# Kernel optimization log

Measured on AMD Instinct MI355X. Metric: run time of the kernel, lower is better.

## Reference

```python
import jax, jax.numpy as jnp
import numpy as np

B, N, H = 2, 2048, 256
NUM_HEADS = 8
HEAD_DIM = H // NUM_HEADS
E = 65536
NEG = -1e30
LN_EPS = 1e-5


def setup_inputs() -> dict:
    key = jax.random.key(0)
    ks = jax.random.split(key, 8)
    x = jax.random.normal(ks[0], (B, N, H), dtype=jnp.float32)
    edge_index = jax.random.randint(ks[1], (2, E), 0, N, dtype=jnp.int32)
    edge_weights = jax.random.uniform(ks[2], (E,), dtype=jnp.float32)
    s = 1.0 / np.sqrt(H)
    Wq = jax.random.normal(ks[3], (H, H), dtype=jnp.float32) * s
    Wk = jax.random.normal(ks[4], (H, H), dtype=jnp.float32) * s
    Wv = jax.random.normal(ks[5], (H, H), dtype=jnp.float32) * s
    Wo = jax.random.normal(ks[6], (H, H), dtype=jnp.float32) * s
    ln_gamma = jnp.ones((H,), dtype=jnp.float32)
    ln_beta = jnp.zeros((H,), dtype=jnp.float32)
    return {"node_embeddings": x, "edge_index": edge_index, "edge_weights": edge_weights,
            "Wq": Wq, "Wk": Wk, "Wv": Wv, "Wo": Wo, "ln_gamma": ln_gamma, "ln_beta": ln_beta}


def reference(node_embeddings, edge_index, edge_weights, Wq, Wk, Wv, Wo, ln_gamma, ln_beta):
    x = node_embeddings
    residual = x
    # torch Linear: y = x @ W.T
    def proj(W):
        y = jnp.einsum('bnd,ed->bne', x, W)
        return y.reshape(B, N, NUM_HEADS, HEAD_DIM).transpose(0, 2, 1, 3)  # [B,h,N,hd]
    Q, K, V = proj(Wq), proj(Wk), proj(Wv)
    scale = 1.0 / jnp.sqrt(jnp.float32(HEAD_DIM))
    scores = jnp.einsum('bhnd,bhmd->bhnm', Q, K) * scale  # [B,h,N,N]
    # adjacency mask from edge list
    mask = jnp.zeros((N, N), dtype=bool).at[edge_index[0], edge_index[1]].set(True)
    scores = jnp.where(mask[None, None], scores, NEG)
    w = jax.nn.softmax(scores, axis=-1)
    # rows with no edges: softmax over uniform NEG -> uniform; multiply by mask zeroes them
    # (equivalent to torch's -inf softmax + nan->0, but grad-safe)
    w = w * mask[None, None].astype(w.dtype)
    attn = jnp.einsum('bhnm,bhmd->bhnd', w, V)
    attn = attn.transpose(0, 2, 1, 3).reshape(B, N, H)
    out = jnp.einsum('bnd,ed->bne', attn, Wo)
    y = out + residual
    mu = jnp.mean(y, axis=-1, keepdims=True)
    var = jnp.mean(jnp.square(y - mu), axis=-1, keepdims=True)
    y = (y - mu) / jnp.sqrt(var + LN_EPS) * ln_gamma + ln_beta
    return y
```

## Files before the change

kernel.cpp:

```cpp
#include <hip/hip_runtime.h>
#include <math.h>

#define Bb 2
#define Nn 2048
#define Hh 256
#define NH 8
#define HD 32
#define NEDGE 65536
#define LN_EPS 1e-5f
#define MW 64

typedef __bf16 bf16_t;
typedef bf16_t bf16x8 __attribute__((ext_vector_type(8)));
typedef bf16_t bf16x4 __attribute__((ext_vector_type(4)));
typedef float f32x4 __attribute__((ext_vector_type(4)));

__global__ void build_mask_kernel(const int* __restrict__ ei, unsigned int* __restrict__ mask) {
    int e = blockIdx.x * blockDim.x + threadIdx.x;
    if (e >= NEDGE) return;
    int src = ei[e];
    int dst = ei[NEDGE + e];
    atomicOr(&mask[src * MW + (dst >> 5)], 1u << (dst & 31));
}

__global__ __launch_bounds__(256) void cvt_zero_kernel(
    const float* __restrict__ s0, const float* __restrict__ s1, const float* __restrict__ s2,
    const float* __restrict__ s3, const float* __restrict__ s4,
    bf16_t* __restrict__ d0, bf16_t* __restrict__ d1, bf16_t* __restrict__ d2,
    bf16_t* __restrict__ d3, bf16_t* __restrict__ d4,
    uint4* __restrict__ mask4)
{
    int which = blockIdx.y;
    int i = blockIdx.x * blockDim.x + threadIdx.x;
    if (which == 5) {
        if (i < Nn * MW / 4) mask4[i] = make_uint4(0, 0, 0, 0);
        return;
    }
    const float* s = (which == 0) ? s0 : (which == 1) ? s1 : (which == 2) ? s2 : (which == 3) ? s3 : s4;
    bf16_t* d = (which == 0) ? d0 : (which == 1) ? d1 : (which == 2) ? d2 : (which == 3) ? d3 : d4;
    int n4 = (which == 0) ? (Bb * Nn * Hh / 4) : (Hh * Hh / 4);
    if (i >= n4) return;
    float4 v = ((const float4*)s)[i];
    bf16x4 o = {(bf16_t)v.x, (bf16_t)v.y, (bf16_t)v.z, (bf16_t)v.w};
    ((bf16x4*)d)[i] = o;
}

#define LDA2 72

__global__ __launch_bounds__(256) void qkv_gemm3_kernel(
    const bf16_t* __restrict__ xb,
    const bf16_t* __restrict__ Wqb, const bf16_t* __restrict__ Wkb, const bf16_t* __restrict__ Wvb,
    float* __restrict__ Qb, bf16_t* __restrict__ Kb16, bf16_t* __restrict__ Vb16)
{
    __shared__ bf16_t As[64 * LDA2];
    __shared__ bf16_t Ws[64 * LDA2];
    int t = threadIdx.x;
    int lane = t & 63, w = t >> 6;
    int wm = w & 1, wn = w >> 1;
    int ml = lane & 15, quad = lane >> 4;
    int m0 = blockIdx.x * 64;
    int wsel = blockIdx.y >> 2;
    const bf16_t* W = (wsel == 0) ? Wqb : ((wsel == 1) ? Wkb : Wvb);
    int n0 = (blockIdx.y & 3) * 64;
    int srow = t >> 3;
    int scol = (t & 7) * 8;
    f32x4 acc[2][2];
    f32x4 zero = {0.f, 0.f, 0.f, 0.f};
    acc[0][0] = zero; acc[0][1] = zero; acc[1][0] = zero; acc[1][1] = zero;

    for (int k0 = 0; k0 < Hh; k0 += 64) {
        bf16x8 a[2], b[2];
        #pragma unroll
        for (int s = 0; s < 2; ++s) {
            a[s] = *(const bf16x8*)(xb + (size_t)(m0 + srow + s * 32) * Hh + k0 + scol);
            b[s] = *(const bf16x8*)(W  + (size_t)(n0 + srow + s * 32) * Hh + k0 + scol);
        }
        __syncthreads();
        #pragma unroll
        for (int s = 0; s < 2; ++s) {
            *(bf16x8*)&As[(srow + s * 32) * LDA2 + scol] = a[s];
            *(bf16x8*)&Ws[(srow + s * 32) * LDA2 + scol] = b[s];
        }
        __syncthreads();
        #pragma unroll
        for (int kk = 0; kk < 64; kk += 32) {
            bf16x8 af[2], bfr[2];
            #pragma unroll
            for (int i = 0; i < 2; ++i) {
                af[i]  = *(const bf16x8*)&As[(wm * 32 + i * 16 + ml) * LDA2 + kk + quad * 8];
                bfr[i] = *(const bf16x8*)&Ws[(wn * 32 + i * 16 + ml) * LDA2 + kk + quad * 8];
            }
            #pragma unroll
            for (int i = 0; i < 2; ++i)
                #pragma unroll
                for (int j = 0; j < 2; ++j)
                    acc[i][j] = __builtin_amdgcn_mfma_f32_16x16x32_bf16(af[i], bfr[j], acc[i][j], 0, 0, 0);
        }
    }
    bf16_t* Ob16 = (wsel == 1) ? Kb16 : Vb16;
    #pragma unroll
    for (int i = 0; i < 2; ++i)
        #pragma unroll
        for (int j = 0; j < 2; ++j)
            #pragma unroll
            for (int r = 0; r < 4; ++r) {
                int mg = m0 + wm * 32 + i * 16 + quad * 4 + r;
                int ng = n0 + wn * 32 + j * 16 + ml;
                float v = acc[i][j][r];
                if (wsel == 0) Qb[(size_t)mg * Hh + ng] = v;
                else           Ob16[(size_t)mg * Hh + ng] = (bf16_t)v;
            }
}

__global__ __launch_bounds__(256) void attn5_kernel(
    const float* __restrict__ Qb, const bf16_t* __restrict__ Kb16, const bf16_t* __restrict__ Vb16,
    const unsigned int* __restrict__ mask, float* __restrict__ attnb)
{
    __shared__ unsigned short nbr[Nn];
    __shared__ float qs[Hh];
    __shared__ float sraw[32 * 9];
    __shared__ float scw[Hh];
    __shared__ float alpha_l[NH];
    __shared__ float linv_l[NH];
    __shared__ float obuf[4][Hh];
    __shared__ int nn_sh;
    int gid = blockIdx.x;
    int i = gid & (Nn - 1);
    int b = gid >> 11;
    int t = threadIdx.x;
    int h = t >> 5, dl = t & 31;
    int w = t >> 6, lane = t & 63;
    int hw = lane >> 3;

    if (t < 64) {
        unsigned int bits = mask[i * MW + t];
        int cnt = __popc(bits);
        int incl = cnt;
        #pragma unroll
        for (int off = 1; off < 64; off <<= 1) {
            int v = __shfl_up(incl, off, 64);
            if (t >= off) incl += v;
        }
        int idx = incl - cnt;
        unsigned int bb = bits;
        while (bb) {
            int bit = __ffs(bb) - 1;
            nbr[idx++] = (unsigned short)(t * 32 + bit);
            bb &= bb - 1;
        }
        if (t == 63) nn_sh = incl;
    }
    qs[t] = Qb[((size_t)((b << 11) + i)) * Hh + t];
    __syncthreads();
    int nn = nn_sh;

    float m_run = -1e30f, l_run = 0.f;
    float o0 = 0.f, o1 = 0.f, o2 = 0.f, o3 = 0.f;
    const float scale = 0.17677669529663687f;
    int nch = (nn + 31) >> 5;
    for (int c = 0; c < nch; ++c) {
        int base = c << 5;
        int lim = min(32, nn - base);
        float4 qv = *(const float4*)&qs[lane << 2];
        #pragma unroll
        for (int s = 0; s < 8; ++s) {
            int r = (s << 2) + w;
            if (r < lim) {
                int j = nbr[base + r];
                bf16x4 kv = *(const bf16x4*)(Kb16 + (((size_t)((b << 11) + j)) << 8) + (lane << 2));
                float p = fmaf((float)kv.x, qv.x, fmaf((float)kv.y, qv.y,
                          fmaf((float)kv.z, qv.z, (float)kv.w * qv.w)));
                p += __shfl_xor(p, 1, 64);
                p += __shfl_xor(p, 2, 64);
                p += __shfl_xor(p, 4, 64);
                if ((lane & 7) == 0) sraw[r * 9 + (lane >> 3)] = p * scale;
            }
        }
        __syncthreads();
        float s_val = (dl < lim) ? sraw[dl * 9 + h] : -1e30f;
        float mc = s_val;
        #pragma unroll
        for (int m = 1; m < 32; m <<= 1) mc = fmaxf(mc, __shfl_xor(mc, m, 64));
        float m_new = fmaxf(m_run, mc);
        float wgt = __expf(s_val - m_new);
        float sum = wgt;
        #pragma unroll
        for (int m = 1; m < 32; m <<= 1) sum += __shfl_xor(sum, m, 64);
        float alpha = __expf(m_run - m_new);
        l_run = l_run * alpha + sum;
        m_run = m_new;
        scw[t] = wgt;
        if (dl == 0) alpha_l[h] = alpha;
        __syncthreads();
        float av = alpha_l[hw];
        o0 *= av; o1 *= av; o2 *= av; o3 *= av;
        #pragma unroll
        for (int s = 0; s < 8; ++s) {
            int r = (s << 2) + w;
            if (r < lim) {
                int j = nbr[base + r];
                float wg = scw[(hw << 5) + r];
                bf16x4 vv = *(const bf16x4*)(Vb16 + (((size_t)((b << 11) + j)) << 8) + (lane << 2));
                o0 = fmaf(wg, (float)vv.x, o0);
                o1 = fmaf(wg, (float)vv.y, o1);
                o2 = fmaf(wg, (float)vv.z, o2);
                o3 = fmaf(wg, (float)vv.w, o3);
            }
        }
    }
    if (dl == 0) linv_l[h] = (l_run > 0.f) ? 1.f / l_run : 0.f;
    obuf[w][(lane << 2) + 0] = o0;
    obuf[w][(lane << 2) + 1] = o1;
    obuf[w][(lane << 2) + 2] = o2;
    obuf[w][(lane << 2) + 3] = o3;
    __syncthreads();
    float val = obuf[0][t] + obuf[1][t] + obuf[2][t] + obuf[3][t];
    attnb[(((size_t)((b << 11) + i)) << 8) + t] = val * linv_l[t >> 5];
}

__global__ __launch_bounds__(256) void out_ln_kernel(
    const float* __restrict__ attnb, const bf16_t* __restrict__ Wob,
    const float* __restrict__ x, const float* __restrict__ gamma,
    const float* __restrict__ beta, float* __restrict__ out)
{
    __shared__ bf16_t As[16 * LDA2];
    __shared__ __align__(16) char wbuf[256 * LDA2 * sizeof(bf16_t)];
    bf16_t* Ws = (bf16_t*)wbuf;
    float* yb = (float*)wbuf;
    int t = threadIdx.x;
    int lane = t & 63, w = t >> 6;
    int ml = lane & 15, quad = lane >> 4;
    int m0 = blockIdx.x * 16;
    f32x4 acc[4];
    f32x4 zero = {0.f, 0.f, 0.f, 0.f};
    acc[0] = zero; acc[1] = zero; acc[2] = zero; acc[3] = zero;
    int arow = t >> 4, acol = (t & 15) * 4;
    int wrow = t >> 3, wcol = (t & 7) * 8;

    for (int k0 = 0; k0 < Hh; k0 += 64) {
        float4 av = *(const float4*)(attnb + (size_t)(m0 + arow) * Hh + k0 + acol);
        bf16x8 wv[8];
        #pragma unroll
        for (int s = 0; s < 8; ++s)
            wv[s] = *(const bf16x8*)(Wob + (size_t)(wrow + s * 32) * Hh + k0 + wcol);
        __syncthreads();
        bf16x4 ac = {(bf16_t)av.x, (bf16_t)av.y, (bf16_t)av.z, (bf16_t)av.w};
        *(bf16x4*)&As[arow * LDA2 + acol] = ac;
        #pragma unroll
        for (int s = 0; s < 8; ++s)
            *(bf16x8*)&Ws[(wrow + s * 32) * LDA2 + wcol] = wv[s];
        __syncthreads();
        #pragma unroll
        for (int kk = 0; kk < 64; kk += 32) {
            bf16x8 af = *(const bf16x8*)&As[ml * LDA2 + kk + quad * 8];
            #pragma unroll
            for (int ct = 0; ct < 4; ++ct) {
                bf16x8 bfr = *(const bf16x8*)&Ws[(w * 64 + ct * 16 + ml) * LDA2 + kk + quad * 8];
                acc[ct] = __builtin_amdgcn_mfma_f32_16x16x32_bf16(af, bfr, acc[ct], 0, 0, 0);
            }
        }
    }
    __syncthreads();
    #pragma unroll
    for (int ct = 0; ct < 4; ++ct)
        #pragma unroll
        for (int r = 0; r < 4; ++r) {
            int row = quad * 4 + r;
            int col = w * 64 + ct * 16 + ml;
            yb[row * 260 + col] = acc[ct][r] + x[(size_t)(m0 + row) * Hh + col];
        }
    __syncthreads();
    for (int rr = 0; rr < 4; ++rr) {
        int row = w * 4 + rr;
        float4 v = *(const float4*)&yb[row * 260 + lane * 4];
        float sum = v.x + v.y + v.z + v.w;
        #pragma unroll
        for (int m = 1; m < 64; m <<= 1) sum += __shfl_xor(sum, m, 64);
        float mu = sum * (1.f / Hh);
        float4 d = {v.x - mu, v.y - mu, v.z - mu, v.w - mu};
        float ss = d.x * d.x + d.y * d.y + d.z * d.z + d.w * d.w;
        #pragma unroll
        for (int m = 1; m < 64; m <<= 1) ss += __shfl_xor(ss, m, 64);
        float r = rsqrtf(ss * (1.f / Hh) + LN_EPS);
        float4 g  = *(const float4*)(gamma + lane * 4);
        float4 bt = *(const float4*)(beta + lane * 4);
        float4 ov = {d.x * r * g.x + bt.x, d.y * r * g.y + bt.y,
                     d.z * r * g.z + bt.z, d.w * r * g.w + bt.w};
        *(float4*)(out + (size_t)(m0 + row) * Hh + lane * 4) = ov;
    }
}

extern "C" void kernel_launch(void* const* d_in, const int* in_sizes, int n_in,
                              void* d_out, int out_size, void* d_ws, size_t ws_size,
                              hipStream_t stream) {
    const float* x     = (const float*)d_in[0];
    const int*   ei    = (const int*)d_in[1];
    const float* Wq    = (const float*)d_in[3];
    const float* Wk    = (const float*)d_in[4];
    const float* Wv    = (const float*)d_in[5];
    const float* Wo    = (const float*)d_in[6];
    const float* gamma = (const float*)d_in[7];
    const float* beta  = (const float*)d_in[8];
    float* out = (float*)d_out;

    const int NTOK = Bb * Nn * Hh;
    float*  Qb    = (float*)d_ws;
    bf16_t* Kb16  = (bf16_t*)(Qb + NTOK);
    bf16_t* Vb16  = Kb16 + NTOK;
    float*  attnb = (float*)(Vb16 + NTOK);
    unsigned int* mask = (unsigned int*)(attnb + NTOK);
    bf16_t* xb  = (bf16_t*)(mask + Nn * MW);
    bf16_t* Wqb = xb + NTOK;
    bf16_t* Wkb = Wqb + Hh * Hh;
    bf16_t* Wvb = Wkb + Hh * Hh;
    bf16_t* Wob = Wvb + Hh * Hh;

    hipLaunchKernelGGL(cvt_zero_kernel, dim3(NTOK / 4 / 256, 6), dim3(256), 0, stream,
                       x, Wq, Wk, Wv, Wo, xb, Wqb, Wkb, Wvb, Wob, (uint4*)mask);
    hipLaunchKernelGGL(build_mask_kernel, dim3(NEDGE / 256), dim3(256), 0, stream, ei, mask);
    hipLaunchKernelGGL(qkv_gemm3_kernel, dim3((Bb * Nn) / 64, 12), dim3(256), 0, stream,
                       xb, Wqb, Wkb, Wvb, Qb, Kb16, Vb16);
    hipLaunchKernelGGL(attn5_kernel, dim3(Bb * Nn), dim3(256), 0, stream,
                       Qb, Kb16, Vb16, mask, attnb);
    hipLaunchKernelGGL(out_ln_kernel, dim3((Bb * Nn) / 16), dim3(256), 0, stream,
                       attnb, Wob, x, gamma, beta, out);
}
```

Measured before the change: 117.4 us.

## Fuse bf16 conversion into GEMMs and process both batches per attention block

Removes the separate fp32-to-bf16 conversion kernel. The QKV and output GEMMs now load fp32 inputs and convert them while staging into shared memory, and the mask is cleared with a memset. The attention kernel now handles both batch elements for a node in one block, so the neighbour list is built once and reused, and the grid is halved. The cost is more registers and shared memory per attention block, and fp32 global loads that are twice as wide inside the GEMMs.

```diff
diff --git a/kernel.cpp b/kernel.cpp
--- a/kernel.cpp
+++ b/kernel.cpp
@@ -23,33 +23,11 @@
     atomicOr(&mask[src * MW + (dst >> 5)], 1u << (dst & 31));
 }
 
-__global__ __launch_bounds__(256) void cvt_zero_kernel(
-    const float* __restrict__ s0, const float* __restrict__ s1, const float* __restrict__ s2,
-    const float* __restrict__ s3, const float* __restrict__ s4,
-    bf16_t* __restrict__ d0, bf16_t* __restrict__ d1, bf16_t* __restrict__ d2,
-    bf16_t* __restrict__ d3, bf16_t* __restrict__ d4,
-    uint4* __restrict__ mask4)
-{
-    int which = blockIdx.y;
-    int i = blockIdx.x * blockDim.x + threadIdx.x;
-    if (which == 5) {
-        if (i < Nn * MW / 4) mask4[i] = make_uint4(0, 0, 0, 0);
-        return;
-    }
-    const float* s = (which == 0) ? s0 : (which == 1) ? s1 : (which == 2) ? s2 : (which == 3) ? s3 : s4;
-    bf16_t* d = (which == 0) ? d0 : (which == 1) ? d1 : (which == 2) ? d2 : (which == 3) ? d3 : d4;
-    int n4 = (which == 0) ? (Bb * Nn * Hh / 4) : (Hh * Hh / 4);
-    if (i >= n4) return;
-    float4 v = ((const float4*)s)[i];
-    bf16x4 o = {(bf16_t)v.x, (bf16_t)v.y, (bf16_t)v.z, (bf16_t)v.w};
-    ((bf16x4*)d)[i] = o;
-}
-
 #define LDA2 72
 
 __global__ __launch_bounds__(256) void qkv_gemm3_kernel(
-    const bf16_t* __restrict__ xb,
-    const bf16_t* __restrict__ Wqb, const bf16_t* __restrict__ Wkb, const bf16_t* __restrict__ Wvb,
+    const float* __restrict__ x,
+    const float* __restrict__ Wq, const float* __restrict__ Wk, const float* __restrict__ Wv,
     float* __restrict__ Qb, bf16_t* __restrict__ Kb16, bf16_t* __restrict__ Vb16)
 {
     __shared__ bf16_t As[64 * LDA2];
@@ -60,7 +38,7 @@
     int ml = lane & 15, quad = lane >> 4;
     int m0 = blockIdx.x * 64;
     int wsel = blockIdx.y >> 2;
-    const bf16_t* W = (wsel == 0) ? Wqb : ((wsel == 1) ? Wkb : Wvb);
+    const float* W = (wsel == 0) ? Wq : ((wsel == 1) ? Wk : Wv);
     int n0 = (blockIdx.y & 3) * 64;
     int srow = t >> 3;
     int scol = (t & 7) * 8;
@@ -69,17 +47,25 @@
     acc[0][0] = zero; acc[0][1] = zero; acc[1][0] = zero; acc[1][1] = zero;
 
     for (int k0 = 0; k0 < Hh; k0 += 64) {
-        bf16x8 a[2], b[2];
+        float4 a[2][2], bwt[2][2];
         #pragma unroll
         for (int s = 0; s < 2; ++s) {
-            a[s] = *(const bf16x8*)(xb + (size_t)(m0 + srow + s * 32) * Hh + k0 + scol);
-            b[s] = *(const bf16x8*)(W  + (size_t)(n0 + srow + s * 32) * Hh + k0 + scol);
+            const float* ap = x + (size_t)(m0 + srow + s * 32) * Hh + k0 + scol;
+            a[s][0] = *(const float4*)ap;
+            a[s][1] = *(const float4*)(ap + 4);
+            const float* bp = W + (size_t)(n0 + srow + s * 32) * Hh + k0 + scol;
+            bwt[s][0] = *(const float4*)bp;
+            bwt[s][1] = *(const float4*)(bp + 4);
         }
         __syncthreads();
         #pragma unroll
         for (int s = 0; s < 2; ++s) {
-            *(bf16x8*)&As[(srow + s * 32) * LDA2 + scol] = a[s];
-            *(bf16x8*)&Ws[(srow + s * 32) * LDA2 + scol] = b[s];
+            bf16x8 av = {(bf16_t)a[s][0].x, (bf16_t)a[s][0].y, (bf16_t)a[s][0].z, (bf16_t)a[s][0].w,
+                         (bf16_t)a[s][1].x, (bf16_t)a[s][1].y, (bf16_t)a[s][1].z, (bf16_t)a[s][1].w};
+            bf16x8 bv = {(bf16_t)bwt[s][0].x, (bf16_t)bwt[s][0].y, (bf16_t)bwt[s][0].z, (bf16_t)bwt[s][0].w,
+                         (bf16_t)bwt[s][1].x, (bf16_t)bwt[s][1].y, (bf16_t)bwt[s][1].z, (bf16_t)bwt[s][1].w};
+            *(bf16x8*)&As[(srow + s * 32) * LDA2 + scol] = av;
+            *(bf16x8*)&Ws[(srow + s * 32) * LDA2 + scol] = bv;
         }
         __syncthreads();
         #pragma unroll
@@ -112,21 +98,19 @@
             }
 }
 
-__global__ __launch_bounds__(256) void attn5_kernel(
+__global__ __launch_bounds__(256) void attn6_kernel(
     const float* __restrict__ Qb, const bf16_t* __restrict__ Kb16, const bf16_t* __restrict__ Vb16,
     const unsigned int* __restrict__ mask, float* __restrict__ attnb)
 {
     __shared__ unsigned short nbr[Nn];
-    __shared__ float qs[Hh];
-    __shared__ float sraw[32 * 9];
-    __shared__ float scw[Hh];
-    __shared__ float alpha_l[NH];
-    __shared__ float linv_l[NH];
+    __shared__ float qs[2][Hh];
+    __shared__ float sraw[2][32 * 9];
+    __shared__ float scw[2][Hh];
+    __shared__ float alpha_l[2][NH];
+    __shared__ float linv_l[2][NH];
     __shared__ float obuf[4][Hh];
     __shared__ int nn_sh;
-    int gid = blockIdx.x;
-    int i = gid & (Nn - 1);
-    int b = gid >> 11;
+    int i = blockIdx.x;
     int t = threadIdx.x;
     int h = t >> 5, dl = t & 31;
     int w = t >> 6, lane = t & 63;
@@ -150,76 +134,94 @@
         }
         if (t == 63) nn_sh = incl;
     }
-    qs[t] = Qb[((size_t)((b << 11) + i)) * Hh + t];
+    qs[0][t] = Qb[(size_t)i * Hh + t];
+    qs[1][t] = Qb[(size_t)(Nn + i) * Hh + t];
     __syncthreads();
     int nn = nn_sh;
 
-    float m_run = -1e30f, l_run = 0.f;
-    float o0 = 0.f, o1 = 0.f, o2 = 0.f, o3 = 0.f;
+    float m_run[2] = {-1e30f, -1e30f};
+    float l_run[2] = {0.f, 0.f};
+    float o[2][4] = {{0.f, 0.f, 0.f, 0.f}, {0.f, 0.f, 0.f, 0.f}};
     const float scale = 0.17677669529663687f;
     int nch = (nn + 31) >> 5;
     for (int c = 0; c < nch; ++c) {
         int base = c << 5;
         int lim = min(32, nn - base);
-        float4 qv = *(const float4*)&qs[lane << 2];
-        #pragma unroll
-        for (int s = 0; s < 8; ++s) {
-            int r = (s << 2) + w;
-            if (r < lim) {
-                int j = nbr[base + r];
-                bf16x4 kv = *(const bf16x4*)(Kb16 + (((size_t)((b << 11) + j)) << 8) + (lane << 2));
-                float p = fmaf((float)kv.x, qv.x, fmaf((float)kv.y, qv.y,
-                          fmaf((float)kv.z, qv.z, (float)kv.w * qv.w)));
-                p += __shfl_xor(p, 1, 64);
-                p += __shfl_xor(p, 2, 64);
-                p += __shfl_xor(p, 4, 64);
-                if ((lane & 7) == 0) sraw[r * 9 + (lane >> 3)] = p * scale;
-            }
-        }
-        __syncthreads();
-        float s_val = (dl < lim) ? sraw[dl * 9 + h] : -1e30f;
-        float mc = s_val;
-        #pragma unroll
-        for (int m = 1; m < 32; m <<= 1) mc = fmaxf(mc, __shfl_xor(mc, m, 64));
-        float m_new = fmaxf(m_run, mc);
-        float wgt = __expf(s_val - m_new);
-        float sum = wgt;
-        #pragma unroll
-        for (int m = 1; m < 32; m <<= 1) sum += __shfl_xor(sum, m, 64);
-        float alpha = __expf(m_run - m_new);
-        l_run = l_run * alpha + sum;
-        m_run = m_new;
-        scw[t] = wgt;
-        if (dl == 0) alpha_l[h] = alpha;
-        __syncthreads();
-        float av = alpha_l[hw];
-        o0 *= av; o1 *= av; o2 *= av; o3 *= av;
-        #pragma unroll
-        for (int s = 0; s < 8; ++s) {
-            int r = (s << 2) + w;
-            if (r < lim) {
-                int j = nbr[base + r];
-                float wg = scw[(hw << 5) + r];
-                bf16x4 vv = *(const bf16x4*)(Vb16 + (((size_t)((b << 11) + j)) << 8) + (lane << 2));
-                o0 = fmaf(wg, (float)vv.x, o0);
-                o1 = fmaf(wg, (float)vv.y, o1);
-                o2 = fmaf(wg, (float)vv.z, o2);
-                o3 = fmaf(wg, (float)vv.w, o3);
-            }
-        }
-    }
-    if (dl == 0) linv_l[h] = (l_run > 0.f) ? 1.f / l_run : 0.f;
-    obuf[w][(lane << 2) + 0] = o0;
-    obuf[w][(lane << 2) + 1] = o1;
-    obuf[w][(lane << 2) + 2] = o2;
-    obuf[w][(lane << 2) + 3] = o3;
-    __syncthreads();
-    float val = obuf[0][t] + obuf[1][t] + obuf[2][t] + obuf[3][t];
-    attnb[(((size_t)((b << 11) + i)) << 8) + t] = val * linv_l[t >> 5];
+        #pragma unroll
+        for (int b = 0; b < 2; ++b) {
+            float4 qv = *(const float4*)&qs[b][lane << 2];
+            #pragma unroll
+            for (int s = 0; s < 8; ++s) {
+                int r = (s << 2) + w;
+                if (r < lim) {
+                    int j = nbr[base + r];
+                    bf16x4 kv = *(const bf16x4*)(Kb16 + (((size_t)((b << 11) + j)) << 8) + (lane << 2));
+                    float p = fmaf((float)kv.x, qv.x, fmaf((float)kv.y, qv.y,
+                              fmaf((float)kv.z, qv.z, (float)kv.w * qv.w)));
+                    p += __shfl_xor(p, 1, 64);
+                    p += __shfl_xor(p, 2, 64);
+                    p += __shfl_xor(p, 4, 64);
+                    if ((lane & 7) == 0) sraw[b][r * 9 + (lane >> 3)] = p * scale;
+                }
+            }
+        }
+        __syncthreads();
+        #pragma unroll
+        for (int b = 0; b < 2; ++b) {
+            float s_val = (dl < lim) ? sraw[b][dl * 9 + h] : -1e30f;
+            float mc = s_val;
+            #pragma unroll
+            for (int m = 1; m < 32; m <<= 1) mc = fmaxf(mc, __shfl_xor(mc, m, 64));
+            float m_new = fmaxf(m_run[b], mc);
+            float wgt = __expf(s_val - m_new);
+            float sum = wgt;
+            #pragma unroll
+            for (int m = 1; m < 32; m <<= 1) sum += __shfl_xor(sum, m, 64);
+            float alpha = __expf(m_run[b] - m_new);
+            l_run[b] = l_run[b] * alpha + sum;
+            m_run[b] = m_new;
+            scw[b][t] = wgt;
+            if (dl == 0) alpha_l[b][h] = alpha;
+        }
+        __syncthreads();
+        #pragma unroll
+        for (int b = 0; b < 2; ++b) {
+            float av = alpha_l[b][hw];
+            o[b][0] *= av; o[b][1] *= av; o[b][2] *= av; o[b][3] *= av;
+            #pragma unroll
+            for (int s = 0; s < 8; ++s) {
+                int r = (s << 2) + w;
+                if (r < lim) {
+                    int j = nbr[base + r];
+                    float wg = scw[b][(hw << 5) + r];
+                    bf16x4 vv = *(const bf16x4*)(Vb16 + (((size_t)((b << 11) + j)) << 8) + (lane << 2));
+                    o[b][0] = fmaf(wg, (float)vv.x, o[b][0]);
+                    o[b][1] = fmaf(wg, (float)vv.y, o[b][1]);
+                    o[b][2] = fmaf(wg, (float)vv.z, o[b][2]);
+                    o[b][3] = fmaf(wg, (float)vv.w, o[b][3]);
+                }
+            }
+        }
+    }
+    if (dl == 0) {
+        linv_l[0][h] = (l_run[0] > 0.f) ? 1.f / l_run[0] : 0.f;
+        linv_l[1][h] = (l_run[1] > 0.f) ? 1.f / l_run[1] : 0.f;
+    }
+    #pragma unroll
+    for (int b = 0; b < 2; ++b) {
+        __syncthreads();
+        obuf[w][(lane << 2) + 0] = o[b][0];
+        obuf[w][(lane << 2) + 1] = o[b][1];
+        obuf[w][(lane << 2) + 2] = o[b][2];
+        obuf[w][(lane << 2) + 3] = o[b][3];
+        __syncthreads();
+        float val = obuf[0][t] + obuf[1][t] + obuf[2][t] + obuf[3][t];
+        attnb[(((size_t)((b << 11) + i)) << 8) + t] = val * linv_l[b][t >> 5];
+    }
 }
 
 __global__ __launch_bounds__(256) void out_ln_kernel(
-    const float* __restrict__ attnb, const bf16_t* __restrict__ Wob,
+    const float* __restrict__ attnb, const float* __restrict__ Wo,
     const float* __restrict__ x, const float* __restrict__ gamma,
     const float* __restrict__ beta, float* __restrict__ out)
 {
@@ -239,16 +241,22 @@
 
     for (int k0 = 0; k0 < Hh; k0 += 64) {
         float4 av = *(const float4*)(attnb + (size_t)(m0 + arow) * Hh + k0 + acol);
-        bf16x8 wv[8];
-        #pragma unroll
-        for (int s = 0; s < 8; ++s)
-            wv[s] = *(const bf16x8*)(Wob + (size_t)(wrow + s * 32) * Hh + k0 + wcol);
+        float4 wva[8], wvb[8];
+        #pragma unroll
+        for (int s = 0; s < 8; ++s) {
+            const float* wp = Wo + (size_t)(wrow + s * 32) * Hh + k0 + wcol;
+            wva[s] = *(const float4*)wp;
+            wvb[s] = *(const float4*)(wp + 4);
+        }
         __syncthreads();
         bf16x4 ac = {(bf16_t)av.x, (bf16_t)av.y, (bf16_t)av.z, (bf16_t)av.w};
         *(bf16x4*)&As[arow * LDA2 + acol] = ac;
         #pragma unroll
-        for (int s = 0; s < 8; ++s)
-            *(bf16x8*)&Ws[(wrow + s * 32) * LDA2 + wcol] = wv[s];
+        for (int s = 0; s < 8; ++s) {
+            bf16x8 wv8 = {(bf16_t)wva[s].x, (bf16_t)wva[s].y, (bf16_t)wva[s].z, (bf16_t)wva[s].w,
+                          (bf16_t)wvb[s].x, (bf16_t)wvb[s].y, (bf16_t)wvb[s].z, (bf16_t)wvb[s].w};
+            *(bf16x8*)&Ws[(wrow + s * 32) * LDA2 + wcol] = wv8;
+        }
         __syncthreads();
         #pragma unroll
         for (int kk = 0; kk < 64; kk += 32) {
@@ -309,19 +317,13 @@
     bf16_t* Vb16  = Kb16 + NTOK;
     float*  attnb = (float*)(Vb16 + NTOK);
     unsigned int* mask = (unsigned int*)(attnb + NTOK);
-    bf16_t* xb  = (bf16_t*)(mask + Nn * MW);
-    bf16_t* Wqb = xb + NTOK;
-    bf16_t* Wkb = Wqb + Hh * Hh;
-    bf16_t* Wvb = Wkb + Hh * Hh;
-    bf16_t* Wob = Wvb + Hh * Hh;
-
-    hipLaunchKernelGGL(cvt_zero_kernel, dim3(NTOK / 4 / 256, 6), dim3(256), 0, stream,
-                       x, Wq, Wk, Wv, Wo, xb, Wqb, Wkb, Wvb, Wob, (uint4*)mask);
+
+    hipMemsetAsync(mask, 0, Nn * MW * sizeof(unsigned int), stream);
     hipLaunchKernelGGL(build_mask_kernel, dim3(NEDGE / 256), dim3(256), 0, stream, ei, mask);
     hipLaunchKernelGGL(qkv_gemm3_kernel, dim3((Bb * Nn) / 64, 12), dim3(256), 0, stream,
-                       xb, Wqb, Wkb, Wvb, Qb, Kb16, Vb16);
-    hipLaunchKernelGGL(attn5_kernel, dim3(Bb * Nn), dim3(256), 0, stream,
+                       x, Wq, Wk, Wv, Qb, Kb16, Vb16);
+    hipLaunchKernelGGL(attn6_kernel, dim3(Nn), dim3(256), 0, stream,
                        Qb, Kb16, Vb16, mask, attnb);
     hipLaunchKernelGGL(out_ln_kernel, dim3((Bb * Nn) / 16), dim3(256), 0, stream,
-                       attnb, Wob, x, gamma, beta, out);
-}
+                       attnb, Wo, x, gamma, beta, out);
+}
```

Measured after the change: 118.6 us. About the same (+1.1%).
